# Kernel tuning notes

Hardware: AMD Instinct MI355X
Metric: run time of the kernel (lower is better)

Reference implementation:

```python
import jax, jax.numpy as jnp
import numpy as np

B = 16384      # batch
CNUM = 2048    # codebook entries
K = 8          # topk
D = 10         # emb_dim
M = 50         # meta_dim
UID = 1000000
IID = 1000000
TAU = 10.0


def setup_inputs() -> dict:
    key = jax.random.key(0)
    ks = jax.random.split(key, 14)
    uid_col = jax.random.randint(ks[0], (B, 1), 0, UID, dtype=jnp.int64)
    iid_col = jax.random.randint(ks[1], (B, 1), 0, IID + 1, dtype=jnp.int64)
    x = jnp.concatenate([uid_col, iid_col], axis=1)
    return {
        "x": x,
        "gumbel_u_src": jax.random.uniform(ks[2], (B, CNUM), dtype=jnp.float32),
        "gumbel_u_tgt": jax.random.uniform(ks[3], (B, CNUM), dtype=jnp.float32),
        "src_uid_table": jax.random.normal(ks[4], (UID, D), dtype=jnp.float32),
        "tgt_uid_table": jax.random.normal(ks[5], (UID, D), dtype=jnp.float32),
        "tgt_iid_table": jax.random.normal(ks[6], (IID + 1, D), dtype=jnp.float32),
        "C": jax.random.normal(ks[7], (CNUM, M), dtype=jnp.float32) * 0.01,
        "w1": jax.random.normal(ks[8], (D, M), dtype=jnp.float32) * 0.01,
        "w2": jax.random.normal(ks[9], (M, D), dtype=jnp.float32) * 0.01,
        "mw1": jax.random.normal(ks[10], (D + M, 50), dtype=jnp.float32) * 0.1,
        "mb1": jnp.zeros((50,), dtype=jnp.float32),
        "mw2": jax.random.normal(ks[11], (50, D * D), dtype=jnp.float32) * 0.1,
        "mb2": jnp.zeros((D * D,), dtype=jnp.float32),
    }


def _gumbel_route(u_emb, C, w1, u_noise):
    # u_emb: [B, D] -> logits s_u: [B, CNUM]
    s = jnp.einsum('bm,cm->bc', u_emb @ w1, C)
    g = -jnp.log(-jnp.log(u_noise + 1e-20) + 1e-20)  # gumbel noise
    gw = jax.nn.softmax((s + g) / TAU, axis=-1)       # F.gumbel_softmax, hard=False
    tw, ti = jax.lax.top_k(gw, K)                     # [B, K]
    c_u = C[ti]                                       # [B, K, M] codebook gather
    return tw, ti, c_u


def reference(x, gumbel_u_src, gumbel_u_tgt, src_uid_table, tgt_uid_table,
              tgt_iid_table, C, w1, w2, mw1, mb1, mw2, mb2):
    # ---- stage == 'test_meta' ----
    # target-side interest embedding ('test_interst' path)
    tuid = tgt_uid_table[x[:, 0]]                      # [B, D]
    tw_t, _, c_t = _gumbel_route(tuid, C, w1, gumbel_u_tgt)
    tuid_ins = ((c_t * tw_t[..., None]).sum(axis=1)) @ w2   # [B, D]
    # source-side routing ('test_meta' path of InterstEmbedding)
    uid = src_uid_table[x[:, 0]]                       # [B, D]
    tw_s, _, c_s = _gumbel_route(uid, C, w1, gumbel_u_src)
    src_fea = jnp.broadcast_to(uid[:, None, :], (uid.shape[0], K, D))  # [B, K, D]
    inp = jnp.concatenate([c_s, src_fea], axis=-1)     # [B, K, M+D] = [B, K, 60]
    h = jax.nn.relu(inp @ mw1 + mb1)                   # [B, K, 50]
    mapping = (h @ mw2 + mb2).reshape(-1, K, D, D)     # per-sample hypernet weights
    src_emb = jnp.einsum('bkd,bkde->bke', src_fea, mapping)  # [B, K, D]
    pre_emb = (src_emb * tw_s[..., None]).sum(axis=1)  # [B, D]
    fin_emb = tuid_ins + pre_emb                       # [B, D]
    iid_emb = tgt_iid_table[x[:, 1]]                   # [B, D]
    return jnp.sum(fin_emb * iid_emb, axis=-1)         # [B]
```

## Files before the change

kernel.cpp:

```cpp
#include <hip/hip_runtime.h>
#include <hip/hip_bf16.h>


#define BROWS 16384
#define CNUM  2048
#define KSEL  8
#define DIMD  10
#define MDIM  50
#define TAUI  0.1f
#define UOFF  832

typedef float    f32x4 __attribute__((ext_vector_type(4)));
typedef _Float16 half8 __attribute__((ext_vector_type(8)));
typedef float    flt2  __attribute__((ext_vector_type(2)));
typedef unsigned int u32;
typedef unsigned long long u64;

__device__ __forceinline__ u32 pkrtz(float a, float b) {
    auto h = __builtin_amdgcn_cvt_pkrtz(a, b);
    union { decltype(h) v; u32 u; } c; c.v = h; return c.u;
}
__device__ __forceinline__ float gnoise(float u) {
    return -__logf(-__logf(u + 1e-20f) + 1e-20f);
}
__device__ __forceinline__ void gload16(const float* g, float* l) {
    __builtin_amdgcn_global_load_lds(
        (const __attribute__((address_space(1))) u32*)g,
        (__attribute__((address_space(3))) u32*)l,
        16, 0, 0);
}

__global__ void cvtC(const float* __restrict__ Cm, u32* __restrict__ C16) {
    const int j = blockIdx.x * 256 + threadIdx.x;
    const int w = j & 3, l = (j >> 2) & 63, pl = (j >> 8) & 1, Tg = j >> 9;
    const int cand = Tg * 16 + (l & 15);
    const int kk = pl * 16 + ((l >> 4) << 2) + w;
    const int k = 2 * kk;
    const float a = (k < MDIM)     ? Cm[cand*MDIM + k]     : 0.f;
    const float b = (k + 1 < MDIM) ? Cm[cand*MDIM + k + 1] : 0.f;
    C16[j] = pkrtz(a, b);
}

__global__ __launch_bounds__(256, 8)
void mf_route(const int* __restrict__ x32,
              const float* __restrict__ gsrc,
              const float* __restrict__ gtgt,
              const float* __restrict__ suid,
              const float* __restrict__ tuid,
              const float* __restrict__ Cm,
              const float* __restrict__ w1,
              const u32* __restrict__ C16,
              float* __restrict__ gTW,
              int*   __restrict__ gTI)
{
    __shared__ __align__(16) float smem[UOFF + 4096];
    __shared__ int sFlag;
    float* sPf  = smem;
    u32*   T48u = (u32*)(smem + 832);
    float* T48l = smem + 1600;
    float* TS   = smem + 2368;

    const int tid  = threadIdx.x;
    const int row0 = blockIdx.x * 8;

    if (tid == 0) sFlag = 1;
    __syncthreads();
    if (tid < 128) { if (x32[2*tid+1] != 0) atomicAnd(&sFlag, 0); }
    __syncthreads();
    const int is64 = sFlag;

    for (int t = tid; t < 16*52; t += 256) {
        const int rt = t / 52, mm = t - rt*52;
        float v = 0.f;
        if (mm < MDIM) {
            const int r = row0 + (rt >> 1);
            const int uidx = is64 ? x32[4*r] : x32[2*r];
            const float* tab = (rt & 1) ? suid : tuid;
            #pragma unroll
            for (int d = 0; d < DIMD; ++d) v += tab[uidx*DIMD + d] * w1[d*MDIM + mm];
        }
        sPf[t] = v;
    }
    __syncthreads();

    const int lane = tid & 63, w = tid >> 6;
    const int lr = lane & 15, lk = lane >> 4;
    const int rt = lr;

    half8 b0, b1;
    {
        union { u32 u[4]; half8 v; } c0, c1;
        #pragma unroll
        for (int jj = 0; jj < 4; ++jj) {
            const int k0 = lk*8 + jj*2;
            c0.u[jj] = pkrtz(sPf[rt*52 + k0], sPf[rt*52 + k0 + 1]);
            const int k1 = 32 + lk*8 + jj*2;
            const float e0 = (k1     < 52) ? sPf[rt*52 + k1]     : 0.f;
            const float e1 = (k1 + 1 < 52) ? sPf[rt*52 + k1 + 1] : 0.f;
            c1.u[jj] = pkrtz(e0, e1);
        }
        b0 = c0.v; b1 = c1.v;
    }

    const int jrow = lane >> 5, jc4 = lane & 31;
    const int rtS0 = 4*w + jrow;
    const int rtS1 = 4*w + 2 + jrow;
    const float* usrc0 = ((rtS0 & 1) ? gsrc : gtgt)
        + (size_t)(row0 + (rtS0 >> 1))*CNUM + ((jc4 ^ (rtS0 & 7)) << 2);
    const float* usrc1 = ((rtS1 & 1) ? gsrc : gtgt)
        + (size_t)(row0 + (rtS1 >> 1))*CNUM + ((jc4 ^ (rtS1 & 7)) << 2);
    float* const udst0a = smem + UOFF +        (4*w    )*128;
    float* const udst1a = smem + UOFF +        (4*w + 2)*128;
    float* const udst0b = smem + UOFF + 2048 + (4*w    )*128;
    float* const udst1b = smem + UOFF + 2048 + (4*w + 2)*128;

    float ts = 0.f;
    float q0=-3.4e38f,q1=-3.4e38f,q2=-3.4e38f,q3=-3.4e38f,
          q4=-3.4e38f,q5=-3.4e38f,q6=-3.4e38f,q7=-3.4e38f;

    const int physa = ((w*8)     + lk) ^ (lr & 7);
    const int physb = ((w*8 + 4) + lk) ^ (lr & 7);
    const int rbase = UOFF + lr*128;

    gload16(usrc0, udst0a);
    gload16(usrc1, udst1a);
    __syncthreads();

    for (int t = 0; t < 16; ++t) {
        const int bufw = (t & 1) * 2048;
        const f32x4 u4a = *(const f32x4*)&smem[rbase + bufw + physa*4];
        const f32x4 u4b = *(const f32x4*)&smem[rbase + bufw + physb*4];
        if (t + 1 < 16) {
            const int nb = ((t + 1) & 1) * 2048;
            gload16(usrc0 + (t + 1)*128, (nb ? udst0b : udst0a));
            gload16(usrc1 + (t + 1)*128, (nb ? udst1b : udst1a));
        }
        #pragma unroll
        for (int nt = 0; nt < 2; ++nt) {
            const int cl = w*32 + nt*16;
            const int Tg = t*8 + w*2 + nt;
            const u32* cp = C16 + (size_t)(Tg*128 + lane)*4;
            const half8 a0 = *(const half8*)cp;
            const half8 a1 = *(const half8*)(cp + 256);
            f32x4 acc = {0.f, 0.f, 0.f, 0.f};
            acc = __builtin_amdgcn_mfma_f32_16x16x32_f16(a0, b0, acc, 0, 0, 0);
            acc = __builtin_amdgcn_mfma_f32_16x16x32_f16(a1, b1, acc, 0, 0, 0);
            const f32x4 u4 = nt ? u4b : u4a;
            const int cg = t*128 + cl + lk*4;
            #pragma unroll
            for (int r4 = 0; r4 < 4; ++r4) {
                const float l = (acc[r4] + gnoise(u4[r4])) * TAUI;
                ts += __expf(l);
                const float xs = __uint_as_float(
                    (__float_as_uint(l) & 0xFFFFF800u) | (u32)(cg + r4));
                q0 = fmaxf(q0, fminf(q1, xs));
                q1 = fmaxf(q1, fminf(q2, xs));
                q2 = fmaxf(q2, fminf(q3, xs));
                q3 = fmaxf(q3, fminf(q4, xs));
                q4 = fmaxf(q4, fminf(q5, xs));
                q5 = fmaxf(q5, fminf(q6, xs));
                q6 = fmaxf(q6, fminf(q7, xs));
                q7 = fmaxf(q7, xs);
            }
        }
        __syncthreads();
    }

    {
        float tss = ts;
        tss += __shfl_xor(tss, 16); tss += __shfl_xor(tss, 32);
        if (lk == 0) TS[rt*4 + w] = tss;
        #pragma unroll
        for (int k = 0; k < 12; ++k) {
            float gm = fmaxf(q7, __shfl_xor(q7, 16));
            gm = fmaxf(gm, __shfl_xor(gm, 32));
            if (q7 == gm) {
                T48u[rt*48 + w*12 + k] = __float_as_uint(q7);
                q7=q6; q6=q5; q5=q4; q4=q3; q3=q2; q2=q1; q1=q0; q0=-3.4e38f;
            }
        }
    }
    __syncthreads();

    for (int e = tid; e < 16*48; e += 256) {
        const int ert = e / 48;
        const int idx = (int)(T48u[e] & 2047u);
        const float* pf = sPf + ert*52;
        const float* cr = Cm + idx*MDIM;
        float s = 0.f;
        #pragma unroll
        for (int k2 = 0; k2 < 25; ++k2) {
            flt2 c = *(const flt2*)(cr + k2*2);
            s += pf[2*k2] * c.x + pf[2*k2+1] * c.y;
        }
        const int r = row0 + (ert >> 1);
        const float u = ((ert & 1) ? gsrc : gtgt)[(size_t)r*CNUM + idx];
        T48l[e] = (s + gnoise(u)) * TAUI;
    }
    __syncthreads();

    if (tid < 16) {
        const int r8 = tid;
        const float inv = 1.0f / (TS[r8*4] + TS[r8*4+1] + TS[r8*4+2] + TS[r8*4+3]);
        u64 used = 0;
        for (int k = 0; k < KSEL; ++k) {
            float bl = -3.4e38f; int bi = 1 << 30; int bj = 0;
            for (int j = 0; j < 48; ++j) {
                if ((used >> j) & 1ull) continue;
                const float lv = T48l[r8*48 + j];
                const int   iv = (int)(T48u[r8*48 + j] & 2047u);
                if (lv > bl || (lv == bl && iv < bi)) { bl = lv; bi = iv; bj = j; }
            }
            used |= 1ull << bj;
            const int grt = blockIdx.x*16 + r8;
            gTW[grt*KSEL + k] = __expf(bl) * inv;
            gTI[grt*KSEL + k] = bi;
        }
    }
}

__global__ __launch_bounds__(256, 4)
void mf_epilog(const int* __restrict__ x32,
               const float* __restrict__ suid,
               const float* __restrict__ tiid,
               const float* __restrict__ Cm,
               const float* __restrict__ w2,
               const float* __restrict__ mw1,
               const float* __restrict__ mb1,
               const float* __restrict__ mw2,
               const float* __restrict__ mb2,
               const float* __restrict__ gTW,
               const int*   __restrict__ gTI,
               float* __restrict__ out)
{
    __shared__ int sFlag;
    const int tid = threadIdx.x;
    const int g = tid >> 4, lg = tid & 15;
    const int row = blockIdx.x * 16 + g;

    if (tid == 0) sFlag = 1;
    __syncthreads();
    if (tid < 128) { if (x32[2*tid+1] != 0) atomicAnd(&sFlag, 0); }
    __syncthreads();
    const int is64 = sFlag;

    const int uidx = is64 ? x32[4*row]     : x32[2*row];
    const int iidx = is64 ? x32[4*row + 2] : x32[2*row + 1];

    float uid[10], ti[10];
    #pragma unroll
    for (int d = 0; d < DIMD; ++d) uid[d] = suid[(size_t)uidx*DIMD + d];
    #pragma unroll
    for (int e = 0; e < DIMD; ++e) ti[e] = tiid[(size_t)iidx*DIMD + e];

    float twt[8], tws[8]; int it[8], is_[8];
    #pragma unroll
    for (int k = 0; k < KSEL; ++k) {
        twt[k] = gTW[(row*2)*KSEL + k];     it[k]  = gTI[(row*2)*KSEL + k];
        tws[k] = gTW[(row*2+1)*KSEL + k];   is_[k] = gTI[(row*2+1)*KSEL + k];
    }

    const int j0 = 4*lg;
    const int nj = (j0 + 4 <= MDIM) ? 4 : (j0 < MDIM ? MDIM - j0 : 0);

    float po = 0.f;
    float qt[4] = {0,0,0,0}, w2t[4] = {0,0,0,0}, hb[4] = {0,0,0,0};

    if (nj) {
        {
            flt2 m0 = *(const flt2*)(mb1 + j0);
            hb[0] = m0.x; hb[1] = m0.y;
            if (nj == 4) { flt2 m1 = *(const flt2*)(mb1 + j0 + 2); hb[2] = m1.x; hb[3] = m1.y; }
            #pragma unroll
            for (int d = 0; d < DIMD; ++d) {
                const float* r = mw1 + (MDIM + d)*MDIM + j0;
                flt2 a = *(const flt2*)r;
                hb[0] += uid[d]*a.x; hb[1] += uid[d]*a.y;
                if (nj == 4) { flt2 b = *(const flt2*)(r + 2); hb[2] += uid[d]*b.x; hb[3] += uid[d]*b.y; }
            }
        }
        for (int jj = 0; jj < nj; ++jj) {
            const float* r = w2 + (j0 + jj)*DIMD;
            float s = 0.f;
            #pragma unroll
            for (int p = 0; p < 5; ++p) { flt2 a = *(const flt2*)(r + 2*p); s += a.x*ti[2*p] + a.y*ti[2*p+1]; }
            w2t[jj] = s;
        }
        for (int jj = 0; jj < nj; ++jj) {
            const float* r = mw2 + (size_t)(j0 + jj)*(DIMD*DIMD);
            float s = 0.f;
            #pragma unroll
            for (int d = 0; d < DIMD; ++d) {
                float sd = 0.f;
                #pragma unroll
                for (int p = 0; p < 5; ++p) { flt2 a = *(const flt2*)(r + d*DIMD + 2*p); sd += a.x*ti[2*p] + a.y*ti[2*p+1]; }
                s += uid[d]*sd;
            }
            qt[jj] = s;
        }
        {
            float ws[4] = {0,0,0,0};
            #pragma unroll
            for (int k = 0; k < KSEL; ++k) {
                const float* cr = Cm + (size_t)it[k]*MDIM + j0;
                flt2 a = *(const flt2*)cr;
                ws[0] += twt[k]*a.x; ws[1] += twt[k]*a.y;
                if (nj == 4) { flt2 b = *(const flt2*)(cr + 2); ws[2] += twt[k]*b.x; ws[3] += twt[k]*b.y; }
            }
            for (int jj = 0; jj < nj; ++jj) po += ws[jj]*w2t[jj];
        }
        float hk[8][4];
        #pragma unroll
        for (int k = 0; k < KSEL; ++k)
            #pragma unroll
            for (int jj = 0; jj < 4; ++jj) hk[k][jj] = hb[jj];
        for (int t2 = 0; t2 < MDIM; t2 += 2) {
            const float* r0 = mw1 + t2*MDIM + j0;
            const float* r1 = mw1 + (t2+1)*MDIM + j0;
            flt2 wa0 = *(const flt2*)r0, wb0 = *(const flt2*)(r0 + 2);
            flt2 wa1 = *(const flt2*)r1, wb1 = *(const flt2*)(r1 + 2);
            #pragma unroll
            for (int k = 0; k < KSEL; ++k) {
                flt2 c = *(const flt2*)(Cm + (size_t)is_[k]*MDIM + t2);
                hk[k][0] += c.x*wa0.x + c.y*wa1.x;
                hk[k][1] += c.x*wa0.y + c.y*wa1.y;
                hk[k][2] += c.x*wb0.x + c.y*wb1.x;
                hk[k][3] += c.x*wb0.y + c.y*wb1.y;
            }
        }
        #pragma unroll
        for (int k = 0; k < KSEL; ++k) {
            float s = 0.f;
            for (int jj = 0; jj < nj; ++jj) s += fmaxf(hk[k][jj], 0.f)*qt[jj];
            po += tws[k]*s;
        }
    }
    if (lg == 0) {
        float stw = 0.f;
        #pragma unroll
        for (int k = 0; k < KSEL; ++k) stw += tws[k];
        float bt = 0.f;
        #pragma unroll
        for (int d = 0; d < DIMD; ++d) {
            float sd = 0.f;
            #pragma unroll
            for (int e = 0; e < DIMD; ++e) sd += mb2[d*DIMD + e]*ti[e];
            bt += uid[d]*sd;
        }
        po += stw*bt;
    }
    po += __shfl_xor(po, 1, 16);
    po += __shfl_xor(po, 2, 16);
    po += __shfl_xor(po, 4, 16);
    po += __shfl_xor(po, 8, 16);
    if (lg == 0) out[row] = po;
}

__global__ __launch_bounds__(256, 4)
void mf_fused_fb(const int* __restrict__ x32,
                 const float* __restrict__ gsrc,
                 const float* __restrict__ gtgt,
                 const float* __restrict__ suid,
                 const float* __restrict__ tuid,
                 const float* __restrict__ tiid,
                 const float* __restrict__ Cm,
                 const float* __restrict__ w1,
                 const float* __restrict__ w2,
                 const float* __restrict__ mw1,
                 const float* __restrict__ mb1,
                 const float* __restrict__ mw2,
                 const float* __restrict__ mb2,
                 float* __restrict__ out)
{
    __shared__ __align__(16) float smem[9536];
    __shared__ int sFlag;
    float* sPf  = smem;
    u32*   T24u = (u32*)(smem + 1664);
    float* T24l = smem + 2432;

    const int tid  = threadIdx.x;
    const int row0 = blockIdx.x * 16;

    if (tid == 0) sFlag = 1;
    __syncthreads();
    if (tid < 128) { if (x32[2*tid+1] != 0) atomicAnd(&sFlag, 0); }
    __syncthreads();
    const int is64 = sFlag;

    for (int t = tid; t < 32*52; t += 256) {
        const int rt = t / 52, mm = t - rt*52;
        float v = 0.f;
        if (mm < MDIM) {
            const int r = row0 + (rt >> 1);
            const int uidx = is64 ? x32[4*r] : x32[2*r];
            const float* tab = (rt & 1) ? suid : tuid;
            #pragma unroll
            for (int d = 0; d < DIMD; ++d) v += tab[uidx*DIMD + d] * w1[d*MDIM + mm];
        }
        sPf[t] = v;
    }
    __syncthreads();

    const int lane = tid & 63, wv = tid >> 6;
    const int lr = lane & 15, lk = lane >> 4;
    const int g = wv & 1, h = wv >> 1;
    const int rt = g*16 + lr;
    const float* up = ((lr & 1) ? gsrc : gtgt) + (size_t)(row0 + g*8 + (lr >> 1)) * CNUM;

    half8 b0, b1;
    {
        union { u32 u[4]; half8 v; } c0, c1;
        #pragma unroll
        for (int jj = 0; jj < 4; ++jj) {
            const int k0 = lk*8 + jj*2;
            c0.u[jj] = pkrtz(sPf[rt*52 + k0], sPf[rt*52 + k0 + 1]);
            const int k1 = 32 + lk*8 + jj*2;
            const float e0 = (k1     < 52) ? sPf[rt*52 + k1]     : 0.f;
            const float e1 = (k1 + 1 < 52) ? sPf[rt*52 + k1 + 1] : 0.f;
            c1.u[jj] = pkrtz(e0, e1);
        }
        b0 = c0.v; b1 = c1.v;
    }

    float ts = 0.f;
    float q0=-3.4e38f,q1=-3.4e38f,q2=-3.4e38f,q3=-3.4e38f,
          q4=-3.4e38f,q5=-3.4e38f,q6=-3.4e38f,q7=-3.4e38f;

    for (int t = 0; t < 64; ++t) {
        const int cb = ((t >> 2) << 7) + h*64 + ((t & 3) << 4);
        const float* cr = Cm + (size_t)(cb + lr)*MDIM;
        union { u32 u[4]; half8 v; } c0, c1;
        #pragma unroll
        for (int jj = 0; jj < 4; ++jj) {
            const int k0 = lk*8 + jj*2;
            c0.u[jj] = pkrtz(cr[k0], cr[k0+1]);
            const int k1 = 32 + lk*8 + jj*2;
            const float e0 = (k1     < MDIM) ? cr[k1]   : 0.f;
            const float e1 = (k1 + 1 < MDIM) ? cr[k1+1] : 0.f;
            c1.u[jj] = pkrtz(e0, e1);
        }
        f32x4 acc = {0.f, 0.f, 0.f, 0.f};
        acc = __builtin_amdgcn_mfma_f32_16x16x32_f16(c0.v, b0, acc, 0, 0, 0);
        acc = __builtin_amdgcn_mfma_f32_16x16x32_f16(c1.v, b1, acc, 0, 0, 0);
        const f32x4 u4 = *(const f32x4*)(up + cb + lk*4);
        const int cg = cb + lk*4;
        #pragma unroll
        for (int r4 = 0; r4 < 4; ++r4) {
            const float l = (acc[r4] + gnoise(u4[r4])) * TAUI;
            ts += __expf(l);
            const float xs = __uint_as_float(
                (__float_as_uint(l) & 0xFFFFF800u) | (u32)(cg + r4));
            q0 = fmaxf(q0, fminf(q1, xs));
            q1 = fmaxf(q1, fminf(q2, xs));
            q2 = fmaxf(q2, fminf(q3, xs));
            q3 = fmaxf(q3, fminf(q4, xs));
            q4 = fmaxf(q4, fminf(q5, xs));
            q5 = fmaxf(q5, fminf(q6, xs));
            q6 = fmaxf(q6, fminf(q7, xs));
            q7 = fmaxf(q7, xs);
        }
    }

    {
        float tss = ts;
        tss += __shfl_xor(tss, 16); tss += __shfl_xor(tss, 32);
        if (lk == 0) smem[3200 + rt*2 + h] = tss;
        #pragma unroll
        for (int k = 0; k < 12; ++k) {
            float gm = fmaxf(q7, __shfl_xor(q7, 16));
            gm = fmaxf(gm, __shfl_xor(gm, 32));
            if (q7 == gm) {
                T24u[rt*24 + h*12 + k] = __float_as_uint(q7);
                q7=q6; q6=q5; q5=q4; q4=q3; q3=q2; q2=q1; q1=q0; q0=-3.4e38f;
            }
        }
    }
    __syncthreads();

    for (int e = tid; e < 32*24; e += 256) {
        const int ert = e / 24;
        const int idx = (int)(T24u[e] & 2047u);
        const float* pf = sPf + ert*52;
        const float* cr = Cm + idx*MDIM;
        float s = 0.f;
        #pragma unroll
        for (int k2 = 0; k2 < 25; ++k2) {
            flt2 c = *(const flt2*)(cr + k2*2);
            s += pf[2*k2] * c.x + pf[2*k2+1] * c.y;
        }
        const int r = row0 + (ert >> 1);
        const float u = ((ert & 1) ? gsrc : gtgt)[(size_t)r*CNUM + idx];
        T24l[e] = (s + gnoise(u)) * TAUI;
    }
    __syncthreads();

    if (tid < 32) {
        const int rrt = tid;
        const float inv = 1.0f / (smem[3200 + rrt*2] + smem[3200 + rrt*2 + 1]);
        u32 used = 0;
        for (int k = 0; k < KSEL; ++k) {
            float bl = -3.4e38f; int bi = 1 << 30; int bj = 0;
            for (int j = 0; j < 24; ++j) {
                if ((used >> j) & 1) continue;
                const float lv = T24l[rrt*24 + j];
                const int   iv = (int)(T24u[rrt*24 + j] & 2047u);
                if (lv > bl || (lv == bl && iv < bi)) { bl = lv; bi = iv; bj = j; }
            }
            used |= 1u << bj;
            smem[8832 + rrt*KSEL + k] = __expf(bl) * inv;
            ((int*)smem)[9088 + rrt*KSEL + k] = bi;
        }
    }
    __syncthreads();

    float* sH    = smem;
    float* sQ    = smem + 832;
    float* sUd   = smem + 9344;
    float* sTopW = smem + 8832;
    int*   sTopI = (int*)smem + 9088;

    const int gg = tid >> 4, lg = tid & 15;
    const int row = row0 + gg;
    const int rt_t = gg*2, rt_s = gg*2 + 1;
    const int uidx = is64 ? x32[4*row]     : x32[2*row];
    const int iidx = is64 ? x32[4*row + 2] : x32[2*row + 1];

    if (lg < DIMD) sUd[gg*12 + lg] = suid[uidx*DIMD + lg];
    __syncthreads();

    for (int t = lg; t < MDIM*DIMD; t += 16) {
        const int j = t / DIMD, e = t - j*DIMD;
        float q = 0.f;
        #pragma unroll
        for (int d = 0; d < DIMD; ++d) q += sUd[gg*12 + d] * mw2[j*(DIMD*DIMD) + d*DIMD + e];
        sQ[gg*500 + t] = q;
    }
    for (int mm = lg; mm < MDIM; mm += 16) {
        float v = 0.f;
        #pragma unroll
        for (int k = 0; k < KSEL; ++k)
            v += sTopW[rt_t*KSEL + k] * Cm[sTopI[rt_t*KSEL + k]*MDIM + mm];
        sH[gg*52 + mm] = v;
    }
    __syncthreads();

    float acc_e = 0.f, be = 0.f;
    if (lg < DIMD) {
        for (int m2 = 0; m2 < MDIM; ++m2) acc_e += sH[gg*52 + m2] * w2[m2*DIMD + lg];
        #pragma unroll
        for (int d = 0; d < DIMD; ++d) be += sUd[gg*12 + d] * mb2[d*DIMD + lg];
    }
    __syncthreads();

    for (int k = 0; k < KSEL; ++k) {
        const int   ik = sTopI[rt_s*KSEL + k];
        const float tw = sTopW[rt_s*KSEL + k];
        for (int j = lg; j < MDIM; j += 16) {
            float hh = mb1[j];
            const float* crow = Cm + ik*MDIM;
            for (int t2 = 0; t2 < MDIM; ++t2) hh += crow[t2] * mw1[t2*MDIM + j];
            #pragma unroll
            for (int d = 0; d < DIMD; ++d) hh += sUd[gg*12 + d] * mw1[(MDIM + d)*MDIM + j];
            sH[gg*52 + j] = fmaxf(hh, 0.f);
        }
        __syncthreads();
        if (lg < DIMD) {
            float se = be;
            for (int j = 0; j < MDIM; ++j) se += sH[gg*52 + j] * sQ[gg*500 + j*DIMD + lg];
            acc_e += tw * se;
        }
        __syncthreads();
    }

    float o = 0.f;
    if (lg < DIMD) o = acc_e * tiid[iidx*DIMD + lg];
    #pragma unroll
    for (int k = 8; k >= 1; k >>= 1) o += __shfl_xor(o, k, 16);
    if (lg == 0) out[row] = o;
}

extern "C" void kernel_launch(void* const* d_in, const int* in_sizes, int n_in,
                              void* d_out, int out_size, void* d_ws, size_t ws_size,
                              hipStream_t stream) {
    (void)in_sizes; (void)n_in; (void)out_size;
    const int*   x32  = (const int*)d_in[0];
    const float* gsrc = (const float*)d_in[1];
    const float* gtgt = (const float*)d_in[2];
    const float* suid = (const float*)d_in[3];
    const float* tuid = (const float*)d_in[4];
    const float* tiid = (const float*)d_in[5];
    const float* Cm   = (const float*)d_in[6];
    const float* w1   = (const float*)d_in[7];
    const float* w2   = (const float*)d_in[8];
    const float* mw1  = (const float*)d_in[9];
    const float* mb1  = (const float*)d_in[10];
    const float* mw2  = (const float*)d_in[11];
    const float* mb2  = (const float*)d_in[12];

    if (ws_size >= 655360u * 4u) {
        u32*   C16 = (u32*)d_ws;
        float* gTW = (float*)d_ws + 131072;
        int*   gTI = (int*)d_ws + 393216;
        hipLaunchKernelGGL(cvtC, dim3(512), dim3(256), 0, stream, Cm, C16);
        hipLaunchKernelGGL(mf_route, dim3(BROWS/8), dim3(256), 0, stream,
                           x32, gsrc, gtgt, suid, tuid, Cm, w1, C16, gTW, gTI);
        hipLaunchKernelGGL(mf_epilog, dim3(BROWS/16), dim3(256), 0, stream,
                           x32, suid, tiid, Cm, w2, mw1, mb1, mw2, mb2, gTW, gTI,
                           (float*)d_out);
    } else {
        hipLaunchKernelGGL(mf_fused_fb, dim3(BROWS/16), dim3(256), 0, stream,
                           x32, gsrc, gtgt, suid, tuid, tiid, Cm, w1, w2, mw1, mb1, mw2, mb2,
                           (float*)d_out);
    }
}
```

Baseline: 278.1 us.

## Precompute gumbel noise as fp16 in swizzled layout via separate prep kernel

Measured after the change: 328.8 us. 1.18x slower.

```diff
diff --git a/kernel.cpp b/kernel.cpp
--- a/kernel.cpp
+++ b/kernel.cpp
@@ -8,7 +8,6 @@
 #define DIMD  10
 #define MDIM  50
 #define TAUI  0.1f
-#define UOFF  832
 
 typedef float    f32x4 __attribute__((ext_vector_type(4)));
 typedef _Float16 half8 __attribute__((ext_vector_type(8)));
@@ -41,6 +40,29 @@
     C16[j] = pkrtz(a, b);
 }
 
+__global__ __launch_bounds__(256)
+void gprep(const float* __restrict__ gsrc,
+           const float* __restrict__ gtgt,
+           u32* __restrict__ NP)
+{
+    const int tid0 = blockIdx.x * 256 + threadIdx.x;
+    for (int i = tid0; i < 16777216; i += 2048*256) {
+        const int s  = i >> 23;
+        const int ri = i & 8388607;
+        const int r  = ri >> 9, c4 = ri & 511;
+        const f32x4 v = ((const f32x4*)(s ? gsrc : gtgt))[ri];
+        const int b = r >> 3, rt = ((r & 7) << 1) + s;
+        const int c = c4 << 2;
+        const int t = c >> 7, gin = (c >> 2) & 31;
+        const int g = gin ^ (rt & 7);
+        const float n0 = gnoise(v[0]), n1 = gnoise(v[1]);
+        const float n2 = gnoise(v[2]), n3 = gnoise(v[3]);
+        u32* dst = NP + (b*16384 + t*1024 + rt*64 + g*2);
+        dst[0] = pkrtz(n0, n1);
+        dst[1] = pkrtz(n2, n3);
+    }
+}
+
 __global__ __launch_bounds__(256, 8)
 void mf_route(const int* __restrict__ x32,
               const float* __restrict__ gsrc,
@@ -50,12 +72,14 @@
               const float* __restrict__ Cm,
               const float* __restrict__ w1,
               const u32* __restrict__ C16,
+              const u32* __restrict__ NP,
               float* __restrict__ gTW,
               int*   __restrict__ gTI)
 {
-    __shared__ __align__(16) float smem[UOFF + 4096];
+    __shared__ __align__(16) float smem[832 + 2048];
     __shared__ int sFlag;
     float* sPf  = smem;
+    u32*   W    = (u32*)smem;
     u32*   T48u = (u32*)(smem + 832);
     float* T48l = smem + 1600;
     float* TS   = smem + 2368;
@@ -102,6 +126,176 @@
         b0 = c0.v; b1 = c1.v;
     }
 
+    const u32* npb = NP + (size_t)blockIdx.x * 16384 + (size_t)lane * 4;
+    float* const udst = smem + 832 + w*256;
+
+    float ts = 0.f;
+    float q0=-3.4e38f,q1=-3.4e38f,q2=-3.4e38f,q3=-3.4e38f,
+          q4=-3.4e38f,q5=-3.4e38f,q6=-3.4e38f,q7=-3.4e38f;
+
+    gload16((const float*)(npb + w*256), udst);
+    __syncthreads();
+
+    for (int t = 0; t < 16; ++t) {
+        const int bufw = (t & 1) * 1024;
+        float nz[2][4];
+        #pragma unroll
+        for (int nt = 0; nt < 2; ++nt) {
+            const int g = w*8 + nt*4 + lk;
+            const int phys = g ^ (lr & 7);
+            const int idx = 832 + bufw + lr*64 + phys*2;
+            union { u32 u[2]; _Float16 h[4]; } nn;
+            nn.u[0] = W[idx]; nn.u[1] = W[idx + 1];
+            #pragma unroll
+            for (int e = 0; e < 4; ++e) nz[nt][e] = (float)nn.h[e];
+        }
+        if (t + 1 < 16)
+            gload16((const float*)(npb + (t + 1)*1024 + w*256),
+                    udst + ((t + 1) & 1)*1024);
+        #pragma unroll
+        for (int nt = 0; nt < 2; ++nt) {
+            const int cl = w*32 + nt*16;
+            const int Tg = t*8 + w*2 + nt;
+            const u32* cp = C16 + (size_t)(Tg*128 + lane)*4;
+            const half8 a0 = *(const half8*)cp;
+            const half8 a1 = *(const half8*)(cp + 256);
+            f32x4 acc = {0.f, 0.f, 0.f, 0.f};
+            acc = __builtin_amdgcn_mfma_f32_16x16x32_f16(a0, b0, acc, 0, 0, 0);
+            acc = __builtin_amdgcn_mfma_f32_16x16x32_f16(a1, b1, acc, 0, 0, 0);
+            const int cg = t*128 + cl + lk*4;
+            #pragma unroll
+            for (int r4 = 0; r4 < 4; ++r4) {
+                const float l = (acc[r4] + nz[nt][r4]) * TAUI;
+                ts += __expf(l);
+                const float xs = __uint_as_float(
+                    (__float_as_uint(l) & 0xFFFFF800u) | (u32)(cg + r4));
+                q0 = fmaxf(q0, fminf(q1, xs));
+                q1 = fmaxf(q1, fminf(q2, xs));
+                q2 = fmaxf(q2, fminf(q3, xs));
+                q3 = fmaxf(q3, fminf(q4, xs));
+                q4 = fmaxf(q4, fminf(q5, xs));
+                q5 = fmaxf(q5, fminf(q6, xs));
+                q6 = fmaxf(q6, fminf(q7, xs));
+                q7 = fmaxf(q7, xs);
+            }
+        }
+        __syncthreads();
+    }
+
+    {
+        float tss = ts;
+        tss += __shfl_xor(tss, 16); tss += __shfl_xor(tss, 32);
+        if (lk == 0) TS[rt*4 + w] = tss;
+        #pragma unroll
+        for (int k = 0; k < 12; ++k) {
+            float gm = fmaxf(q7, __shfl_xor(q7, 16));
+            gm = fmaxf(gm, __shfl_xor(gm, 32));
+            if (q7 == gm) {
+                T48u[rt*48 + w*12 + k] = __float_as_uint(q7);
+                q7=q6; q6=q5; q5=q4; q4=q3; q3=q2; q2=q1; q1=q0; q0=-3.4e38f;
+            }
+        }
+    }
+    __syncthreads();
+
+    for (int e = tid; e < 16*48; e += 256) {
+        const int ert = e / 48;
+        const int idx = (int)(T48u[e] & 2047u);
+        const float* pf = sPf + ert*52;
+        const float* cr = Cm + idx*MDIM;
+        float s = 0.f;
+        #pragma unroll
+        for (int k2 = 0; k2 < 25; ++k2) {
+            flt2 c = *(const flt2*)(cr + k2*2);
+            s += pf[2*k2] * c.x + pf[2*k2+1] * c.y;
+        }
+        const int r = row0 + (ert >> 1);
+        const float u = ((ert & 1) ? gsrc : gtgt)[(size_t)r*CNUM + idx];
+        T48l[e] = (s + gnoise(u)) * TAUI;
+    }
+    __syncthreads();
+
+    if (tid < 16) {
+        const int r8 = tid;
+        const float inv = 1.0f / (TS[r8*4] + TS[r8*4+1] + TS[r8*4+2] + TS[r8*4+3]);
+        u64 used = 0;
+        for (int k = 0; k < KSEL; ++k) {
+            float bl = -3.4e38f; int bi = 1 << 30; int bj = 0;
+            for (int j = 0; j < 48; ++j) {
+                if ((used >> j) & 1ull) continue;
+                const float lv = T48l[r8*48 + j];
+                const int   iv = (int)(T48u[r8*48 + j] & 2047u);
+                if (lv > bl || (lv == bl && iv < bi)) { bl = lv; bi = iv; bj = j; }
+            }
+            used |= 1ull << bj;
+            const int grt = blockIdx.x*16 + r8;
+            gTW[grt*KSEL + k] = __expf(bl) * inv;
+            gTI[grt*KSEL + k] = bi;
+        }
+    }
+}
+
+__global__ __launch_bounds__(256, 8)
+void mf_route_r8(const int* __restrict__ x32,
+                 const float* __restrict__ gsrc,
+                 const float* __restrict__ gtgt,
+                 const float* __restrict__ suid,
+                 const float* __restrict__ tuid,
+                 const float* __restrict__ Cm,
+                 const float* __restrict__ w1,
+                 const u32* __restrict__ C16,
+                 float* __restrict__ gTW,
+                 int*   __restrict__ gTI)
+{
+    __shared__ __align__(16) float smem[832 + 4096];
+    __shared__ int sFlag;
+    float* sPf  = smem;
+    u32*   T48u = (u32*)(smem + 832);
+    float* T48l = smem + 1600;
+    float* TS   = smem + 2368;
+
+    const int tid  = threadIdx.x;
+    const int row0 = blockIdx.x * 8;
+
+    if (tid == 0) sFlag = 1;
+    __syncthreads();
+    if (tid < 128) { if (x32[2*tid+1] != 0) atomicAnd(&sFlag, 0); }
+    __syncthreads();
+    const int is64 = sFlag;
+
+    for (int t = tid; t < 16*52; t += 256) {
+        const int rt = t / 52, mm = t - rt*52;
+        float v = 0.f;
+        if (mm < MDIM) {
+            const int r = row0 + (rt >> 1);
+            const int uidx = is64 ? x32[4*r] : x32[2*r];
+            const float* tab = (rt & 1) ? suid : tuid;
+            #pragma unroll
+            for (int d = 0; d < DIMD; ++d) v += tab[uidx*DIMD + d] * w1[d*MDIM + mm];
+        }
+        sPf[t] = v;
+    }
+    __syncthreads();
+
+    const int lane = tid & 63, w = tid >> 6;
+    const int lr = lane & 15, lk = lane >> 4;
+    const int rt = lr;
+
+    half8 b0, b1;
+    {
+        union { u32 u[4]; half8 v; } c0, c1;
+        #pragma unroll
+        for (int jj = 0; jj < 4; ++jj) {
+            const int k0 = lk*8 + jj*2;
+            c0.u[jj] = pkrtz(sPf[rt*52 + k0], sPf[rt*52 + k0 + 1]);
+            const int k1 = 32 + lk*8 + jj*2;
+            const float e0 = (k1     < 52) ? sPf[rt*52 + k1]     : 0.f;
+            const float e1 = (k1 + 1 < 52) ? sPf[rt*52 + k1 + 1] : 0.f;
+            c1.u[jj] = pkrtz(e0, e1);
+        }
+        b0 = c0.v; b1 = c1.v;
+    }
+
     const int jrow = lane >> 5, jc4 = lane & 31;
     const int rtS0 = 4*w + jrow;
     const int rtS1 = 4*w + 2 + jrow;
@@ -109,10 +303,10 @@
         + (size_t)(row0 + (rtS0 >> 1))*CNUM + ((jc4 ^ (rtS0 & 7)) << 2);
     const float* usrc1 = ((rtS1 & 1) ? gsrc : gtgt)
         + (size_t)(row0 + (rtS1 >> 1))*CNUM + ((jc4 ^ (rtS1 & 7)) << 2);
-    float* const udst0a = smem + UOFF +        (4*w    )*128;
-    float* const udst1a = smem + UOFF +        (4*w + 2)*128;
-    float* const udst0b = smem + UOFF + 2048 + (4*w    )*128;
-    float* const udst1b = smem + UOFF + 2048 + (4*w + 2)*128;
+    float* const udst0a = smem + 832 +        (4*w    )*128;
+    float* const udst1a = smem + 832 +        (4*w + 2)*128;
+    float* const udst0b = smem + 832 + 2048 + (4*w    )*128;
+    float* const udst1b = smem + 832 + 2048 + (4*w + 2)*128;
 
     float ts = 0.f;
     float q0=-3.4e38f,q1=-3.4e38f,q2=-3.4e38f,q3=-3.4e38f,
@@ -120,7 +314,7 @@
 
     const int physa = ((w*8)     + lk) ^ (lr & 7);
     const int physb = ((w*8 + 4) + lk) ^ (lr & 7);
-    const int rbase = UOFF + lr*128;
+    const int rbase = 832 + lr*128;
 
     gload16(usrc0, udst0a);
     gload16(usrc1, udst1a);
@@ -597,12 +791,25 @@
     const float* mw2  = (const float*)d_in[11];
     const float* mb2  = (const float*)d_in[12];
 
-    if (ws_size >= 655360u * 4u) {
+    const size_t NEED_FULL = (655360ull + 33554432ull) * 4ull;
+    if (ws_size >= NEED_FULL) {
+        u32*   C16 = (u32*)d_ws;
+        float* gTW = (float*)d_ws + 131072;
+        int*   gTI = (int*)d_ws + 393216;
+        u32*   NP  = (u32*)d_ws + 655360;
+        hipLaunchKernelGGL(cvtC, dim3(512), dim3(256), 0, stream, Cm, C16);
+        hipLaunchKernelGGL(gprep, dim3(2048), dim3(256), 0, stream, gsrc, gtgt, NP);
+        hipLaunchKernelGGL(mf_route, dim3(BROWS/8), dim3(256), 0, stream,
+                           x32, gsrc, gtgt, suid, tuid, Cm, w1, C16, NP, gTW, gTI);
+        hipLaunchKernelGGL(mf_epilog, dim3(BROWS/16), dim3(256), 0, stream,
+                           x32, suid, tiid, Cm, w2, mw1, mb1, mw2, mb2, gTW, gTI,
+                           (float*)d_out);
+    } else if (ws_size >= 655360u * 4u) {
         u32*   C16 = (u32*)d_ws;
         float* gTW = (float*)d_ws + 131072;
         int*   gTI = (int*)d_ws + 393216;
         hipLaunchKernelGGL(cvtC, dim3(512), dim3(256), 0, stream, Cm, C16);
-        hipLaunchKernelGGL(mf_route, dim3(BROWS/8), dim3(256), 0, stream,
+        hipLaunchKernelGGL(mf_route_r8, dim3(BROWS/8), dim3(256), 0, stream,
                            x32, gsrc, gtgt, suid, tuid, Cm, w1, C16, gTW, gTI);
         hipLaunchKernelGGL(mf_epilog, dim3(BROWS/16), dim3(256), 0, stream,
                            x32, suid, tiid, Cm, w2, mw1, mb1, mw2, mb2, gTW, gTI,
```
